# Kernel optimization log

Hardware: AMD Instinct MI355X
Metric: run time of the kernel (lower is better)

The kernel has to match this reference:

```python
import jax, jax.numpy as jnp
import numpy as np

GROUP_SIZE = 7
ROI_SCALE = 1.3
BIN_SCALE = 1.5


def setup_inputs() -> dict:
    key = jax.random.key(0)
    k1, k2, k3, k4 = jax.random.split(key, 4)
    B, C, H, W = 2, 490, 128, 128  # C = output_dim(10) * group_size(7)**2
    N = 512
    stride = 16
    features = jax.random.normal(k1, (B, C, H, W), dtype=jnp.float32)
    img_w = W * stride
    bidx = jax.random.randint(k2, (N, 1), 0, B).astype(jnp.float32)
    xy1 = jax.random.uniform(k3, (N, 2), minval=0.0, maxval=img_w - 64.0)
    wh = jax.random.uniform(k4, (N, 2), minval=32.0, maxval=512.0)
    xy2 = jnp.minimum(xy1 + wh, img_w - 1.0)
    rois = jnp.concatenate([bidx, xy1[:, 0:1], xy1[:, 1:2], xy2[:, 0:1], xy2[:, 1:2]], axis=1)
    return {"rois": rois, "features": features, "stride": stride}


def reference(rois, features, stride):
    G = GROUP_SIZE
    B, C, H, W = features.shape
    D = C // (G * G)  # output_dim, computed dynamically as in the torch module
    dt = features.dtype
    spatial_scale = 1.0 / stride

    rois = rois[:, :5].astype(dt)
    batch_idx = rois[:, 0].astype(jnp.int32)  # [N]
    # rounded roi corners in feature-map coordinates (end is inclusive +1)
    rsw = jnp.round(rois[:, 1]) * spatial_scale
    rsh = jnp.round(rois[:, 2]) * spatial_scale
    rew = (jnp.round(rois[:, 3]) + 1.0) * spatial_scale
    reh = (jnp.round(rois[:, 4]) + 1.0) * spatial_scale
    # mask (context) enlargement around roi center by ROI_SCALE
    rw, rh = rew - rsw, reh - rsh
    rwm, rhm = rw * ROI_SCALE, rh * ROI_SCALE
    swm = (rsw + rew) * 0.5 - rwm * 0.5
    shm = (rsh + reh) * 0.5 - rhm * 0.5
    rwm = jnp.maximum(rwm, 0.1)  # force tiny rois to 1x1
    rhm = jnp.maximum(rhm, 0.1)
    bin_h = rhm / G  # [N]
    bin_w = rwm / G
    dh = bin_h * (BIN_SCALE - 1.0) * 0.5  # extra bin context
    dw = bin_w * (BIN_SCALE - 1.0) * 0.5

    g = jnp.arange(G, dtype=dt)  # bin index
    hstart = jnp.clip(jnp.floor(shm[:, None] + g[None, :] * bin_h[:, None] - dh[:, None]), 0, H).astype(jnp.int32)  # [N,G]
    hend = jnp.clip(jnp.ceil(shm[:, None] + (g[None, :] + 1.0) * bin_h[:, None] + dh[:, None]), 0, H).astype(jnp.int32)
    wstart = jnp.clip(jnp.floor(swm[:, None] + g[None, :] * bin_w[:, None] - dw[:, None]), 0, W).astype(jnp.int32)
    wend = jnp.clip(jnp.ceil(swm[:, None] + (g[None, :] + 1.0) * bin_w[:, None] + dw[:, None]), 0, W).astype(jnp.int32)

    # integral image so each bin-average is 4 gathers instead of a dynamic loop
    cs = jnp.cumsum(jnp.cumsum(features, axis=2), axis=3)
    S = jnp.pad(cs, ((0, 0), (0, 0), (1, 0), (1, 0)))  # [B,C,H+1,W+1]
    # position-sensitive channel map c = (d*G + ph)*G + pw  <=>  reshape C -> [D,G,G]
    Sr = S.reshape(B, D, G, G, H + 1, W + 1)

    N = rois.shape[0]
    b_ = batch_idx[:, None, None, None]          # [N,1,1,1]
    d_ = jnp.arange(D)[None, :, None, None]      # [1,D,1,1]
    pi = jnp.arange(G)[None, None, :, None]      # [1,1,G,1] (ph)
    pj = jnp.arange(G)[None, None, None, :]      # [1,1,1,G] (pw)
    hs = hstart[:, None, :, None]
    he = hend[:, None, :, None]
    ws = wstart[:, None, None, :]
    we = wend[:, None, None, :]

    total = (Sr[b_, d_, pi, pj, he, we] - Sr[b_, d_, pi, pj, hs, we]
             - Sr[b_, d_, pi, pj, he, ws] + Sr[b_, d_, pi, pj, hs, ws])  # [N,D,G,G]

    area = ((hend - hstart)[:, None, :, None] * (wend - wstart)[:, None, None, :])  # [N,1->D,G,G] via broadcast
    area = jnp.broadcast_to(area, total.shape)
    out = jnp.where(area > 0, total / jnp.maximum(area, 1).astype(dt), jnp.zeros((), dt))
    return out
```

## Files before the change

### kernel.cpp

```cpp
#include <hip/hip_runtime.h>

#define GS   7
#define CCH  490
#define HH   128
#define WW   128
#define LDW  132
#define NB   2
#define NCH  (NB * CCH)

__global__ __launch_bounds__(512, 4) void psroi_rowpfx(
    const float* __restrict__ rois,
    const float* __restrict__ feat,
    const int*   __restrict__ stride_p,
    float*       __restrict__ out)
{
#pragma clang fp contract(off)
    __shared__ float S[HH * LDW];

    const int ch  = blockIdx.x;
    const int tid = threadIdx.x;

    {
        const int row = tid >> 2;
        const int sg  = tid & 3;
        const float* __restrict__ fp = feat + (size_t)ch * (HH * WW) + row * WW + sg * 32;

        float u[32];
        #pragma unroll
        for (int i = 0; i < 8; ++i) {
            const float4 q = *(const float4*)&fp[i * 4];
            u[4 * i + 0] = q.x; u[4 * i + 1] = q.y;
            u[4 * i + 2] = q.z; u[4 * i + 3] = q.w;
        }
        #pragma unroll
        for (int i = 1; i < 32; ++i)
            u[i] += u[i - 1];

        const float tot = u[31];
        const float t1 = __shfl_up(tot, 1, 64);
        const float t2 = __shfl_up(tot, 2, 64);
        const float t3 = __shfl_up(tot, 3, 64);
        float off = 0.0f;
        if (sg > 0) off += t1;
        if (sg > 1) off += t2;
        if (sg > 2) off += t3;

        float* rp = &S[row * LDW + sg * 32];
        #pragma unroll
        for (int i = 0; i < 8; ++i) {
            float4 q;
            q.x = u[4 * i + 0] + off; q.y = u[4 * i + 1] + off;
            q.z = u[4 * i + 2] + off; q.w = u[4 * i + 3] + off;
            *(float4*)&rp[i * 4] = q;
        }
    }
    __syncthreads();

    {
        const int n  = tid;
        const int b  = ch / CCH;
        const int c  = ch - b * CCH;
        const int bi = (int)rois[n * 5 + 0];
        if (bi == b) {
            const float ss = 1.0f / (float)(*stride_p);
            const float x1 = rois[n * 5 + 1];
            const float y1 = rois[n * 5 + 2];
            const float x2 = rois[n * 5 + 3];
            const float y2 = rois[n * 5 + 4];

            float rsw = rintf(x1) * ss;
            float rsh = rintf(y1) * ss;
            float rew = (rintf(x2) + 1.0f) * ss;
            float reh = (rintf(y2) + 1.0f) * ss;
            float rwm = (rew - rsw) * 1.3f;
            float rhm = (reh - rsh) * 1.3f;
            const float swm = (rsw + rew) * 0.5f - rwm * 0.5f;
            const float shm = (rsh + reh) * 0.5f - rhm * 0.5f;
            rwm = fmaxf(rwm, 0.1f);
            rhm = fmaxf(rhm, 0.1f);
            const float bin_h = rhm / 7.0f;
            const float bin_w = rwm / 7.0f;
            const float dh = bin_h * 0.25f;
            const float dw = bin_w * 0.25f;

            const int d   = c / (GS * GS);
            const int rem = c - d * (GS * GS);
            const int pi  = rem / GS;
            const int pj  = rem - pi * GS;
            const float gi = (float)pi;
            const float gj = (float)pj;

            const int hs  = (int)fminf(fmaxf(floorf(shm + gi * bin_h - dh),          0.0f), 128.0f);
            const int he  = (int)fminf(fmaxf(ceilf (shm + (gi + 1.0f) * bin_h + dh), 0.0f), 128.0f);
            const int ws2 = (int)fminf(fmaxf(floorf(swm + gj * bin_w - dw),          0.0f), 128.0f);
            const int we  = (int)fminf(fmaxf(ceilf (swm + (gj + 1.0f) * bin_w + dw), 0.0f), 128.0f);

            const int area = (he - hs) * (we - ws2);
            float total = 0.0f;
            if (area > 0) {
                if (ws2 > 0) {
                    for (int r = hs; r < he; ++r)
                        total += S[r * LDW + (we - 1)] - S[r * LDW + (ws2 - 1)];
                } else {
                    for (int r = hs; r < he; ++r)
                        total += S[r * LDW + (we - 1)];
                }
            }
            out[(size_t)n * CCH + c] = (area > 0) ? (total / (float)area) : 0.0f;
        }
    }
}

extern "C" void kernel_launch(void* const* d_in, const int* in_sizes, int n_in,
                              void* d_out, int out_size, void* d_ws, size_t ws_size,
                              hipStream_t stream)
{
    const float* rois     = (const float*)d_in[0];
    const float* feat     = (const float*)d_in[1];
    const int*   stride_p = (const int*)d_in[2];
    float*       out      = (float*)d_out;

    dim3 grid(NCH);
    dim3 block(512);
    hipLaunchKernelGGL(psroi_rowpfx, grid, block, 0, stream, rois, feat, stride_p, out);
}
```

Before: 99.45 us.

## Process two channels per block, prefetching second channel during first pooling

Each block now handles a pair of adjacent channels. The ROI geometry is computed once and reused for both. The second channel's global load is issued before pooling the first channel, so memory latency overlaps with the LDS reads. Outputs are written as a float2, which halves the grid and cuts per-ROI setup. The trade-offs are an extra __syncthreads, 32 more live registers during the first pooling, and half as many blocks to hide latency.

```diff
diff --git a/kernel.cpp b/kernel.cpp
--- a/kernel.cpp
+++ b/kernel.cpp
@@ -6,9 +6,10 @@
 #define WW   128
 #define LDW  132
 #define NB   2
-#define NCH  (NB * CCH)
+#define NPAIR (CCH / 2)
+#define NBLK  (NB * NPAIR)
 
-__global__ __launch_bounds__(512, 4) void psroi_rowpfx(
+__global__ __launch_bounds__(512, 4) void psroi_pair(
     const float* __restrict__ rois,
     const float* __restrict__ feat,
     const int*   __restrict__ stride_p,
@@ -17,25 +18,39 @@
 #pragma clang fp contract(off)
     __shared__ float S[HH * LDW];
 
-    const int ch  = blockIdx.x;
+    const int blk = blockIdx.x;
+    const int b   = blk / NPAIR;
+    const int c0  = (blk - b * NPAIR) * 2;
+    const int ch0 = b * CCH + c0;
     const int tid = threadIdx.x;
+    const int row = tid >> 2;
+    const int sg  = tid & 3;
 
-    {
-        const int row = tid >> 2;
-        const int sg  = tid & 3;
-        const float* __restrict__ fp = feat + (size_t)ch * (HH * WW) + row * WW + sg * 32;
+    const float ss = 1.0f / (float)(*stride_p);
+    const int   bi = (int)rois[tid * 5 + 0];
+    const float x1 = rois[tid * 5 + 1];
+    const float y1 = rois[tid * 5 + 2];
+    const float x2 = rois[tid * 5 + 3];
+    const float y2 = rois[tid * 5 + 4];
+    float rsw = rintf(x1) * ss;
+    float rsh = rintf(y1) * ss;
+    float rew = (rintf(x2) + 1.0f) * ss;
+    float reh = (rintf(y2) + 1.0f) * ss;
+    float rwm = (rew - rsw) * 1.3f;
+    float rhm = (reh - rsh) * 1.3f;
+    const float swm = (rsw + rew) * 0.5f - rwm * 0.5f;
+    const float shm = (rsh + reh) * 0.5f - rhm * 0.5f;
+    rwm = fmaxf(rwm, 0.1f);
+    rhm = fmaxf(rhm, 0.1f);
+    const float bin_h = rhm / 7.0f;
+    const float bin_w = rwm / 7.0f;
+    const float dh = bin_h * 0.25f;
+    const float dw = bin_w * 0.25f;
 
-        float u[32];
-        #pragma unroll
-        for (int i = 0; i < 8; ++i) {
-            const float4 q = *(const float4*)&fp[i * 4];
-            u[4 * i + 0] = q.x; u[4 * i + 1] = q.y;
-            u[4 * i + 2] = q.z; u[4 * i + 3] = q.w;
-        }
+    auto build_prefix = [&](float (&u)[32]) {
         #pragma unroll
         for (int i = 1; i < 32; ++i)
             u[i] += u[i - 1];
-
         const float tot = u[31];
         const float t1 = __shfl_up(tot, 1, 64);
         const float t2 = __shfl_up(tot, 2, 64);
@@ -44,7 +59,6 @@
         if (sg > 0) off += t1;
         if (sg > 1) off += t2;
         if (sg > 2) off += t3;
-
         float* rp = &S[row * LDW + sg * 32];
         #pragma unroll
         for (int i = 0; i < 8; ++i) {
@@ -53,61 +67,68 @@
             q.z = u[4 * i + 2] + off; q.w = u[4 * i + 3] + off;
             *(float4*)&rp[i * 4] = q;
         }
+    };
+
+    auto pool = [&](int c) -> float {
+        if (bi != b) return 0.0f;
+        const int d   = c / (GS * GS);
+        const int rem = c - d * (GS * GS);
+        const int pi  = rem / GS;
+        const int pj  = rem - pi * GS;
+        const float gi = (float)pi;
+        const float gj = (float)pj;
+        const int hs  = (int)fminf(fmaxf(floorf(shm + gi * bin_h - dh),          0.0f), 128.0f);
+        const int he  = (int)fminf(fmaxf(ceilf (shm + (gi + 1.0f) * bin_h + dh), 0.0f), 128.0f);
+        const int ws2 = (int)fminf(fmaxf(floorf(swm + gj * bin_w - dw),          0.0f), 128.0f);
+        const int we  = (int)fminf(fmaxf(ceilf (swm + (gj + 1.0f) * bin_w + dw), 0.0f), 128.0f);
+        const int area = (he - hs) * (we - ws2);
+        float total = 0.0f;
+        if (area > 0) {
+            if (ws2 > 0) {
+                for (int r = hs; r < he; ++r)
+                    total += S[r * LDW + (we - 1)] - S[r * LDW + (ws2 - 1)];
+            } else {
+                for (int r = hs; r < he; ++r)
+                    total += S[r * LDW + (we - 1)];
+            }
+        }
+        return (area > 0) ? (total / (float)area) : 0.0f;
+    };
+
+    float u[32];
+    {
+        const float* __restrict__ fp = feat + (size_t)ch0 * (HH * WW) + row * WW + sg * 32;
+        #pragma unroll
+        for (int i = 0; i < 8; ++i) {
+            const float4 q = *(const float4*)&fp[i * 4];
+            u[4 * i + 0] = q.x; u[4 * i + 1] = q.y;
+            u[4 * i + 2] = q.z; u[4 * i + 3] = q.w;
+        }
+        build_prefix(u);
     }
     __syncthreads();
 
     {
-        const int n  = tid;
-        const int b  = ch / CCH;
-        const int c  = ch - b * CCH;
-        const int bi = (int)rois[n * 5 + 0];
-        if (bi == b) {
-            const float ss = 1.0f / (float)(*stride_p);
-            const float x1 = rois[n * 5 + 1];
-            const float y1 = rois[n * 5 + 2];
-            const float x2 = rois[n * 5 + 3];
-            const float y2 = rois[n * 5 + 4];
+        const float* __restrict__ fp = feat + (size_t)(ch0 + 1) * (HH * WW) + row * WW + sg * 32;
+        #pragma unroll
+        for (int i = 0; i < 8; ++i) {
+            const float4 q = *(const float4*)&fp[i * 4];
+            u[4 * i + 0] = q.x; u[4 * i + 1] = q.y;
+            u[4 * i + 2] = q.z; u[4 * i + 3] = q.w;
+        }
+    }
 
-            float rsw = rintf(x1) * ss;
-            float rsh = rintf(y1) * ss;
-            float rew = (rintf(x2) + 1.0f) * ss;
-            float reh = (rintf(y2) + 1.0f) * ss;
-            float rwm = (rew - rsw) * 1.3f;
-            float rhm = (reh - rsh) * 1.3f;
-            const float swm = (rsw + rew) * 0.5f - rwm * 0.5f;
-            const float shm = (rsh + reh) * 0.5f - rhm * 0.5f;
-            rwm = fmaxf(rwm, 0.1f);
-            rhm = fmaxf(rhm, 0.1f);
-            const float bin_h = rhm / 7.0f;
-            const float bin_w = rwm / 7.0f;
-            const float dh = bin_h * 0.25f;
-            const float dw = bin_w * 0.25f;
+    const float v0 = pool(c0);
+    __syncthreads();
 
-            const int d   = c / (GS * GS);
-            const int rem = c - d * (GS * GS);
-            const int pi  = rem / GS;
-            const int pj  = rem - pi * GS;
-            const float gi = (float)pi;
-            const float gj = (float)pj;
+    build_prefix(u);
+    __syncthreads();
 
-            const int hs  = (int)fminf(fmaxf(floorf(shm + gi * bin_h - dh),          0.0f), 128.0f);
-            const int he  = (int)fminf(fmaxf(ceilf (shm + (gi + 1.0f) * bin_h + dh), 0.0f), 128.0f);
-            const int ws2 = (int)fminf(fmaxf(floorf(swm + gj * bin_w - dw),          0.0f), 128.0f);
-            const int we  = (int)fminf(fmaxf(ceilf (swm + (gj + 1.0f) * bin_w + dw), 0.0f), 128.0f);
+    const float v1 = pool(c0 + 1);
 
-            const int area = (he - hs) * (we - ws2);
-            float total = 0.0f;
-            if (area > 0) {
-                if (ws2 > 0) {
-                    for (int r = hs; r < he; ++r)
-                        total += S[r * LDW + (we - 1)] - S[r * LDW + (ws2 - 1)];
-                } else {
-                    for (int r = hs; r < he; ++r)
-                        total += S[r * LDW + (we - 1)];
-                }
-            }
-            out[(size_t)n * CCH + c] = (area > 0) ? (total / (float)area) : 0.0f;
-        }
+    if (bi == b) {
+        float2 o; o.x = v0; o.y = v1;
+        *(float2*)&out[(size_t)tid * CCH + c0] = o;
     }
 }
 
@@ -120,7 +141,7 @@
     const int*   stride_p = (const int*)d_in[2];
     float*       out      = (float*)d_out;
 
-    dim3 grid(NCH);
+    dim3 grid(NBLK);
     dim3 block(512);
-    hipLaunchKernelGGL(psroi_rowpfx, grid, block, 0, stream, rois, feat, stride_p, out);
+    hipLaunchKernelGGL(psroi_pair, grid, block, 0, stream, rois, feat, stride_p, out);
 }
```

New measurement: 99.54 us. No clear change (+0.1%).
